# Optimization experiments

Measured on AMD Instinct MI355X. Metric: run time of the kernel, lower is better.

The kernel has to match this reference:

```python
import jax, jax.numpy as jnp
import numpy as np

N = 100000
E = 1600000
D = 128


def setup_inputs() -> dict:
    key = jax.random.key(0)
    k1, k2, k3 = jax.random.split(key, 3)
    indices = jax.random.randint(k1, (2, E), 0, N, dtype=jnp.int64)
    values = jax.random.normal(k2, (E,), dtype=jnp.float32)
    b = jax.random.normal(k3, (N, D), dtype=jnp.float32)
    return {"indices": indices, "values": values, "n": N, "b": b}


def reference(indices, values, n, b):
    # Sparse COO SpMM: out[r] = sum_{e: row[e]==r} values[e] * b[col[e]]
    row, col = indices[0], indices[1]
    contrib = values[:, None] * b[col]          # [E, D] gather-multiply
    out = jax.ops.segment_sum(contrib, row, num_segments=n)  # [N, D] scatter-add
    return out
```

## Files before the change

kernel.cpp:

```cpp
#include <hip/hip_runtime.h>
#include <hip/hip_fp16.h>


#define D_DIM 128
#define RPB 64
#define RPB_SHIFT 6
#define CRB 256
#define CRB_SHIFT 8
#define MAXCB 512
#define CCAP 4608
#define MAXB 2048
#define CAP_LDS 1408
#define EPT 6
#define EPT1 8
#define CHUNK1 4096
#define EPC 4
#define OVF_T 8192

typedef float fx4 __attribute__((ext_vector_type(4)));

__global__ __launch_bounds__(256) void convert_b_kernel(
        const float* __restrict__ b, __half* __restrict__ bh, int n8) {
    int i = blockIdx.x * blockDim.x + threadIdx.x;
    if (i >= n8) return;
    const float4* b4 = (const float4*)b;
    float4 a0 = b4[2 * i];
    float4 a1 = b4[2 * i + 1];
    union { __half2 h[4]; uint4 u; } pk;
    pk.h[0] = __floats2half2_rn(a0.x, a0.y);
    pk.h[1] = __floats2half2_rn(a0.z, a0.w);
    pk.h[2] = __floats2half2_rn(a1.x, a1.y);
    pk.h[3] = __floats2half2_rn(a1.z, a1.w);
    ((uint4*)bh)[i] = pk.u;
}

__global__ __launch_bounds__(1024) void p1_sortcoarse(
        const int* __restrict__ rows,
        const int* __restrict__ cols,
        const float* __restrict__ vals,
        int* __restrict__ coarse_cnt,
        int2* __restrict__ coarse,
        int* __restrict__ ovf_cnt,
        int* __restrict__ ovf3,
        int E, int ncb, int ccap) {
    __shared__ int hist[MAXCB];
    __shared__ int cursor[MAXCB];
    __shared__ int2 stage[CHUNK1];
    __shared__ unsigned short sbkt[CHUNK1];

    int tid = threadIdx.x;
    int start = blockIdx.x * CHUNK1;
    int end = start + CHUNK1; if (end > E) end = E;
    int n = end - start;

    for (int i = tid; i < ncb; i += 1024) hist[i] = 0;
    __syncthreads();

    int rr[EPC]; int cc[EPC]; float vv[EPC];
    int ne = 0;
    for (int e = start + tid; e < end; e += 1024) {
        int r = rows[e];
        if (ne < EPC) { rr[ne] = r; cc[ne] = cols[e]; vv[ne] = vals[e]; }
        ++ne;
        atomicAdd(&hist[r >> CRB_SHIFT], 1);
    }
    __syncthreads();

    for (int d = 1; d < ncb; d <<= 1) {
        int t = (tid < ncb && tid >= d) ? hist[tid - d] : 0;
        __syncthreads();
        if (tid < ncb && tid >= d) hist[tid] += t;
        __syncthreads();
    }

    int incl = 0, excl = 0;
    if (tid < ncb) { incl = hist[tid]; excl = tid ? hist[tid - 1] : 0; }
    __syncthreads();
    if (tid < ncb) {
        int cnt = incl - excl;
        cursor[tid] = excl;
        int gres = (cnt > 0) ? atomicAdd(&coarse_cnt[tid], cnt) : 0;
        hist[tid] = gres - excl;
    }
    __syncthreads();

    for (int j = 0; j < ne; ++j) {
        int r, c; float v;
        if (j < EPC) { r = rr[j]; c = cc[j]; v = vv[j]; }
        else { int e = start + tid + j * 1024; r = rows[e]; c = cols[e]; v = vals[e]; }
        int bkt = r >> CRB_SHIFT;
        int pos = atomicAdd(&cursor[bkt], 1);
        stage[pos] = make_int2(((r & (CRB - 1)) << 17) | c, __float_as_int(v));
        sbkt[pos] = (unsigned short)bkt;
    }
    __syncthreads();

    for (int i = tid; i < n; i += 1024) {
        int bkt = sbkt[i];
        int2 e = stage[i];
        int gidx = i + hist[bkt];
        if (gidx < ccap) {
            coarse[(size_t)bkt * ccap + gidx] = e;
        } else {
            int k = atomicAdd(ovf_cnt, 1);
            if (k < OVF_T) {
                int r = (bkt << CRB_SHIFT) | ((unsigned)e.x >> 17);
                ovf3[3 * k] = r; ovf3[3 * k + 1] = e.x & 0x1FFFF;
                ovf3[3 * k + 2] = e.y;
            }
        }
    }
}

__global__ __launch_bounds__(1024) void p2_fine(
        const int* __restrict__ coarse_cnt,
        const int2* __restrict__ coarse,
        int* __restrict__ bucket_cnt,
        int2* __restrict__ packed,
        int* __restrict__ ovf_cnt,
        int* __restrict__ ovf3,
        int ccap, int cap, int nb) {
    __shared__ int2 stage[CCAP];
    __shared__ int hist4[4];
    __shared__ int loff[5];
    __shared__ int cur[4];

    int bin = blockIdx.x;
    int tid = threadIdx.x;
    int lane = tid & 63;
    int cnt = coarse_cnt[bin];
    if (cnt > ccap) cnt = ccap;
    const int2* cb = coarse + (size_t)bin * ccap;

    if (tid < 4) hist4[tid] = 0;

    int h0 = 0, h1 = 0, h2 = 0, h3 = 0;
    for (int i = tid; i < cnt; i += 1024) {
        int f = (cb[i].x >> 23) & 3;
        h0 += (f == 0); h1 += (f == 1); h2 += (f == 2); h3 += (f == 3);
    }
    for (int off = 32; off; off >>= 1) {
        h0 += __shfl_down(h0, off); h1 += __shfl_down(h1, off);
        h2 += __shfl_down(h2, off); h3 += __shfl_down(h3, off);
    }
    __syncthreads();
    if (lane == 0) {
        atomicAdd(&hist4[0], h0); atomicAdd(&hist4[1], h1);
        atomicAdd(&hist4[2], h2); atomicAdd(&hist4[3], h3);
    }
    __syncthreads();
    if (tid == 0) {
        int o = 0;
        for (int k = 0; k < 4; ++k) { loff[k] = o; cur[k] = o; o += hist4[k]; }
        loff[4] = o;
    }
    __syncthreads();

    for (int i = tid; i < cnt; i += 1024) {
        int2 e = cb[i];
        int f = (e.x >> 23) & 3;
        int p = 0;
        for (int k = 0; k < 4; ++k) {
            unsigned long long m = __ballot(f == k);
            if (f == k) {
                int leader = __ffsll((unsigned long long)m) - 1;
                int base = 0;
                if (lane == leader) base = atomicAdd(&cur[k], (int)__popcll(m));
                base = __shfl(base, leader);
                p = base + (int)__popcll(m & ((1ULL << lane) - 1ULL));
            }
        }
        stage[p] = e;
    }
    __syncthreads();

    int fb0 = bin << (CRB_SHIFT - RPB_SHIFT);
    for (int k = 0; k < 4; ++k) {
        int bkt = fb0 + k;
        if (bkt >= nb) break;
        int s = loff[k];
        int run = loff[k + 1] - s;
        int w = (run > cap) ? cap : run;
        for (int i = tid; i < w; i += 1024) {
            int2 e = stage[s + i];
            packed[(size_t)bkt * cap + i] = make_int2(e.x & 0x7FFFFF, e.y);
        }
        if (tid == 0) bucket_cnt[bkt] = w;
        for (int i = cap + tid; i < run; i += 1024) {
            int2 e = stage[s + i];
            int k2 = atomicAdd(ovf_cnt, 1);
            if (k2 < OVF_T) {
                int r = (bin << CRB_SHIFT) | ((unsigned)e.x >> 17);
                ovf3[3 * k2] = r; ovf3[3 * k2 + 1] = e.x & 0x1FFFF;
                ovf3[3 * k2 + 2] = e.y;
            }
        }
    }
}

template <bool HALF>
__global__ __launch_bounds__(256) void phase2_sort_gather(
        const int* __restrict__ bucket_cnt,
        const int2* __restrict__ packed,
        const __half* __restrict__ bh,
        const float* __restrict__ b,
        float* __restrict__ out,
        int cap, int N) {
    __shared__ int2 sorted[CAP_LDS];
    __shared__ int hist[RPB];
    __shared__ int offs[RPB + 1];
    __shared__ int cursor[RPB];

    int bucket = blockIdx.x;
    int tid = threadIdx.x;

    int cnt = bucket_cnt[bucket];
    if (cnt > cap) cnt = cap;
    const int2* pk = packed + (size_t)bucket * cap;

    if (tid < RPB) hist[tid] = 0;
    __syncthreads();

    int2 ev[EPT];
    int  rl[EPT];
    int ne = 0;
    for (int i = tid; i < cnt; i += 256) {
        int2 e = pk[i];
        ev[ne] = e;
        rl[ne] = ((unsigned)e.x) >> 17;
        atomicAdd(&hist[rl[ne]], 1);
        ++ne;
    }
    __syncthreads();

    for (int d = 1; d < RPB; d <<= 1) {
        int t = (tid < RPB && tid >= d) ? hist[tid - d] : 0;
        __syncthreads();
        if (tid < RPB) hist[tid] += t;
        __syncthreads();
    }
    if (tid == 0) offs[0] = 0;
    if (tid < RPB) {
        offs[tid + 1] = hist[tid];
        cursor[tid] = (tid == 0) ? 0 : hist[tid - 1];
    }
    __syncthreads();

    for (int j = 0; j < ne; ++j) {
        int pos = atomicAdd(&cursor[rl[j]], 1);
        sorted[pos] = make_int2(ev[j].x & 0x1FFFF, ev[j].y);
    }
    __syncthreads();

    int g = tid >> 5;
    int glane = tid & 31;
    int r0 = bucket << RPB_SHIFT;
    for (int k = 0; k < 8; ++k) {
        int rr = g * 8 + k;
        int start = offs[rr];
        int num = offs[rr + 1] - start;
        float4 acc = make_float4(0.f, 0.f, 0.f, 0.f);
        for (int base = 0; base < num; base += 8) {
#pragma unroll
            for (int j = 0; j < 8; ++j) {
                int idx = base + j;
                int sidx = start + ((idx < num) ? idx : (num - 1));
                int2 e = sorted[sidx];
                float v = (idx < num) ? __int_as_float(e.y) : 0.f;
                if (HALF) {
                    uint2 hv = ((const uint2*)(bh + (size_t)e.x * D_DIM))[glane];
                    __half2* hp = (__half2*)&hv;
                    float2 f0 = __half22float2(hp[0]);
                    float2 f1 = __half22float2(hp[1]);
                    acc.x += v * f0.x;
                    acc.y += v * f0.y;
                    acc.z += v * f1.x;
                    acc.w += v * f1.y;
                } else {
                    float4 bv = ((const float4*)(b + (size_t)e.x * D_DIM))[glane];
                    acc.x += v * bv.x;
                    acc.y += v * bv.y;
                    acc.z += v * bv.z;
                    acc.w += v * bv.w;
                }
            }
        }
        int r = r0 + rr;
        if (r < N) {
            fx4 av = {acc.x, acc.y, acc.z, acc.w};
            __builtin_nontemporal_store(av, (fx4*)(out + (size_t)r * D_DIM) + glane);
        }
    }
}

__global__ __launch_bounds__(1024) void phase1_partition(
        const int* __restrict__ rows,
        const int* __restrict__ cols,
        const float* __restrict__ vals,
        int* __restrict__ bucket_cnt,
        int2* __restrict__ packed,
        int* __restrict__ ovf_cnt,
        int* __restrict__ ovf3,
        int E, int nb, int cap, int chunk) {
    __shared__ int hist[MAXB];
    int tid = threadIdx.x;
    int start = blockIdx.x * chunk;
    int end = start + chunk; if (end > E) end = E;

    for (int i = tid; i < nb; i += 1024) hist[i] = 0;
    __syncthreads();

    int rr[EPT1]; int cc[EPT1]; float vv[EPT1];
    int ne = 0;
    for (int e = start + tid; e < end; e += 1024) {
        int r = rows[e];
        if (ne < EPT1) { rr[ne] = r; cc[ne] = cols[e]; vv[ne] = vals[e]; }
        ++ne;
        atomicAdd(&hist[r >> RPB_SHIFT], 1);
    }
    __syncthreads();

    for (int bkt = tid; bkt < nb; bkt += 1024) {
        int c = hist[bkt];
        hist[bkt] = (c > 0) ? atomicAdd(&bucket_cnt[bkt], c) : 0;
    }
    __syncthreads();

    int j = 0;
    for (int e = start + tid; e < end; e += 1024, ++j) {
        int r, c; float v;
        if (j < EPT1) { r = rr[j]; c = cc[j]; v = vv[j]; }
        else          { r = rows[e]; c = cols[e]; v = vals[e]; }
        int bkt = r >> RPB_SHIFT;
        int local = atomicAdd(&hist[bkt], 1);
        if (local < cap) {
            int key = ((r & (RPB - 1)) << 17) | c;
            packed[(size_t)bkt * cap + local] = make_int2(key, __float_as_int(v));
        } else {
            int k = atomicAdd(ovf_cnt, 1);
            if (k < OVF_T) {
                ovf3[3 * k] = r; ovf3[3 * k + 1] = c;
                ovf3[3 * k + 2] = __float_as_int(v);
            }
        }
    }
}

__global__ void fixup_kernel(const int* __restrict__ ovf_cnt,
                             const int* __restrict__ ovf3,
                             const float* __restrict__ b,
                             float* __restrict__ out) {
    int items = *ovf_cnt;
    if (items > OVF_T) items = OVF_T;
    int gsz  = (gridDim.x * blockDim.x) >> 5;
    int gid  = (blockIdx.x * blockDim.x + threadIdx.x) >> 5;
    int lane = threadIdx.x & 31;
    for (int i = gid; i < items; i += gsz) {
        int r = ovf3[3 * i];
        int c = ovf3[3 * i + 1];
        float v = __int_as_float(ovf3[3 * i + 2]);
        float4 bv = ((const float4*)(b + (size_t)c * D_DIM))[lane];
        float* op = out + (size_t)r * D_DIM + (size_t)lane * 4;
        atomicAdd(op + 0, v * bv.x);
        atomicAdd(op + 1, v * bv.y);
        atomicAdd(op + 2, v * bv.z);
        atomicAdd(op + 3, v * bv.w);
    }
}

__global__ void spmm_atomic_kernel(const int* __restrict__ rows,
                                   const int* __restrict__ cols,
                                   const float* __restrict__ vals,
                                   const float* __restrict__ b,
                                   float* __restrict__ out, int E) {
    int t = blockIdx.x * blockDim.x + threadIdx.x;
    int e = t >> 5;
    if (e >= E) return;
    int lane = t & 31;
    int r = rows[e];
    int c = cols[e];
    float v = vals[e];
    float4 bv = ((const float4*)(b + (size_t)c * D_DIM))[lane];
    float* op = out + (size_t)r * D_DIM + (size_t)lane * 4;
    atomicAdd(op + 0, v * bv.x);
    atomicAdd(op + 1, v * bv.y);
    atomicAdd(op + 2, v * bv.z);
    atomicAdd(op + 3, v * bv.w);
}

extern "C" void kernel_launch(void* const* d_in, const int* in_sizes, int n_in,
                              void* d_out, int out_size, void* d_ws, size_t ws_size,
                              hipStream_t stream) {
    const int*   indices = (const int*)d_in[0];
    const float* vals    = (const float*)d_in[1];
    const float* b       = (const float*)d_in[3];
    float*       out     = (float*)d_out;

    int E = in_sizes[1];
    int N = out_size / D_DIM;
    const int* rows = indices;
    const int* cols = indices + E;

    int nb  = (N + RPB - 1) >> RPB_SHIFT;
    int ncb = (N + CRB - 1) >> CRB_SHIFT;
    int avg  = (nb  > 0) ? E / nb  : 0;
    int cavg = (ncb > 0) ? E / ncb : 0;
    int cap = CAP_LDS;
    size_t bh_bytes = (size_t)N * D_DIM * 2;
    int n8 = N * D_DIM / 8;

    {
        bool ok = (ncb <= MAXCB) && (N <= 131072) &&
                  (cavg + cavg / 8 <= CCAP) && (cap > avg + avg / 8);
        size_t fixedN = (size_t)ncb * 4 + (size_t)nb * 4 + 4 + (size_t)OVF_T * 12;
        size_t pk_off = (fixedN + 255) & ~(size_t)255;
        size_t un_off = (pk_off + (size_t)nb * cap * 8 + 255) & ~(size_t)255;
        size_t coarse_bytes = (size_t)ncb * CCAP * 8;
        size_t un_bytes = coarse_bytes > bh_bytes ? coarse_bytes : bh_bytes;
        if (ok && ws_size >= un_off + un_bytes) {
            char* w = (char*)d_ws;
            int*    coarse_cnt = (int*)w;
            int*    bucket_cnt = (int*)(w + (size_t)ncb * 4);
            int*    ovf_cnt    = (int*)(w + (size_t)ncb * 4 + (size_t)nb * 4);
            int*    ovf3       = (int*)(w + (size_t)ncb * 4 + (size_t)nb * 4 + 4);
            int2*   packed     = (int2*)(w + pk_off);
            int2*   coarse     = (int2*)(w + un_off);
            __half* bh         = (__half*)(w + un_off);

            (void)hipMemsetAsync(coarse_cnt, 0,
                                 (size_t)ncb * 4 + (size_t)nb * 4 + 4, stream);

            int nwg1 = (E + CHUNK1 - 1) / CHUNK1;
            p1_sortcoarse<<<nwg1, 1024, 0, stream>>>(
                rows, cols, vals, coarse_cnt, coarse, ovf_cnt, ovf3,
                E, ncb, CCAP);

            p2_fine<<<ncb, 1024, 0, stream>>>(
                coarse_cnt, coarse, bucket_cnt, packed, ovf_cnt, ovf3,
                CCAP, cap, nb);

            convert_b_kernel<<<(n8 + 255) / 256, 256, 0, stream>>>(b, bh, n8);

            phase2_sort_gather<true><<<nb, 256, 0, stream>>>(
                bucket_cnt, packed, bh, b, out, cap, N);

            fixup_kernel<<<8, 256, 0, stream>>>(ovf_cnt, ovf3, b, out);
            return;
        }
    }

    size_t fixed      = (size_t)nb * 4 + 4 + (size_t)OVF_T * 12;
    size_t bh_off     = (fixed + 255) & ~(size_t)255;
    size_t packed_h   = (bh_off + bh_bytes + 255) & ~(size_t)255;
    size_t packed_f   = bh_off;
    size_t need_h     = packed_h + (size_t)nb * cap * 8;
    size_t need_f     = packed_f + (size_t)nb * cap * 8;

    bool okBase = (nb <= MAXB) && (N <= 131072) && (cap > avg + avg / 8);
    bool useHalf = okBase && (ws_size >= need_h);
    bool useF32  = okBase && !useHalf && (ws_size >= need_f);

    if (!useHalf && !useF32) {
        (void)hipMemsetAsync(d_out, 0, (size_t)out_size * sizeof(float), stream);
        long long total = (long long)E * 32;
        int blocks = (int)((total + 255) / 256);
        spmm_atomic_kernel<<<blocks, 256, 0, stream>>>(rows, cols, vals, b, out, E);
        return;
    }

    char* w = (char*)d_ws;
    int*    bucket_cnt = (int*)w;
    int*    ovf_cnt    = (int*)(w + (size_t)nb * 4);
    int*    ovf3       = (int*)(w + (size_t)nb * 4 + 4);
    __half* bh         = (__half*)(w + bh_off);
    int2*   packed     = (int2*)(w + (useHalf ? packed_h : packed_f));

    (void)hipMemsetAsync(bucket_cnt, 0, (size_t)nb * 4 + 4, stream);

    if (useHalf)
        convert_b_kernel<<<(n8 + 255) / 256, 256, 0, stream>>>(b, bh, n8);

    const int P1_WGS = 256;
    int chunk = (E + P1_WGS - 1) / P1_WGS;
    phase1_partition<<<P1_WGS, 1024, 0, stream>>>(
        rows, cols, vals, bucket_cnt, packed, ovf_cnt, ovf3, E, nb, cap, chunk);

    if (useHalf)
        phase2_sort_gather<true><<<nb, 256, 0, stream>>>(
            bucket_cnt, packed, bh, b, out, cap, N);
    else
        phase2_sort_gather<false><<<nb, 256, 0, stream>>>(
            bucket_cnt, packed, bh, b, out, cap, N);

    fixup_kernel<<<8, 256, 0, stream>>>(ovf_cnt, ovf3, b, out);
}
```

Measured before the change: 216.9 us.

## Sort coarse bins into per-row CSR in place and gather rows directly

```diff
diff --git a/kernel.cpp b/kernel.cpp
--- a/kernel.cpp
+++ b/kernel.cpp
@@ -15,6 +15,7 @@
 #define EPT1 8
 #define CHUNK1 4096
 #define EPC 4
+#define EPC2 5
 #define OVF_T 8192
 
 typedef float fx4 __attribute__((ext_vector_type(4)));
@@ -112,87 +113,164 @@
     }
 }
 
-__global__ __launch_bounds__(1024) void p2_fine(
+__global__ __launch_bounds__(1024) void p2_rowsort(
         const int* __restrict__ coarse_cnt,
-        const int2* __restrict__ coarse,
+        int2* __restrict__ coarse,
+        int* __restrict__ row_beg,
+        int* __restrict__ row_num,
+        int ccap, int N) {
+    __shared__ int2 stage[CCAP];
+    __shared__ int hist[CRB];
+    __shared__ int offs[CRB + 1];
+    __shared__ int cursor[CRB];
+
+    int bin = blockIdx.x;
+    int tid = threadIdx.x;
+    int cnt = coarse_cnt[bin];
+    if (cnt > ccap) cnt = ccap;
+    int2* cb = coarse + (size_t)bin * ccap;
+
+    if (tid < CRB) hist[tid] = 0;
+    __syncthreads();
+
+    int2 ev[EPC2];
+    int  rl[EPC2];
+    int ne = 0;
+    for (int i = tid; i < cnt; i += 1024) {
+        int2 e = cb[i];
+        ev[ne] = e;
+        rl[ne] = ((unsigned)e.x) >> 17;
+        atomicAdd(&hist[rl[ne]], 1);
+        ++ne;
+    }
+    __syncthreads();
+
+    for (int d = 1; d < CRB; d <<= 1) {
+        int t = (tid < CRB && tid >= d) ? hist[tid - d] : 0;
+        __syncthreads();
+        if (tid < CRB) hist[tid] += (tid >= d) ? t : 0;
+        __syncthreads();
+    }
+    if (tid == 0) offs[0] = 0;
+    if (tid < CRB) {
+        offs[tid + 1] = hist[tid];
+        cursor[tid] = (tid == 0) ? 0 : hist[tid - 1];
+    }
+    __syncthreads();
+
+    for (int j = 0; j < ne; ++j) {
+        int pos = atomicAdd(&cursor[rl[j]], 1);
+        stage[pos] = make_int2(ev[j].x & 0x1FFFF, ev[j].y);
+    }
+    __syncthreads();
+
+    for (int i = tid; i < cnt; i += 1024) cb[i] = stage[i];
+    if (tid < CRB) {
+        int r = (bin << CRB_SHIFT) + tid;
+        if (r < N) {
+            row_beg[r] = bin * ccap + offs[tid];
+            row_num[r] = offs[tid + 1] - offs[tid];
+        }
+    }
+}
+
+template <bool HALF>
+__global__ __launch_bounds__(256) void csr_gather(
+        const int* __restrict__ row_beg,
+        const int* __restrict__ row_num,
+        const int2* __restrict__ csr,
+        const __half* __restrict__ bh,
+        const float* __restrict__ b,
+        float* __restrict__ out,
+        int N) {
+    int g = threadIdx.x >> 5;
+    int glane = threadIdx.x & 31;
+    int r = blockIdx.x * 8 + g;
+    if (r >= N) return;
+
+    int beg = row_beg[r];
+    int num = row_num[r];
+    const int2* pk = csr + beg;
+
+    float4 acc = make_float4(0.f, 0.f, 0.f, 0.f);
+    for (int base = 0; base < num; base += 8) {
+#pragma unroll
+        for (int j = 0; j < 8; ++j) {
+            int idx = base + j;
+            int sidx = (idx < num) ? idx : (num - 1);
+            int2 e = pk[sidx];
+            float v = (idx < num) ? __int_as_float(e.y) : 0.f;
+            if (HALF) {
+                uint2 hv = ((const uint2*)(bh + (size_t)e.x * D_DIM))[glane];
+                __half2* hp = (__half2*)&hv;
+                float2 f0 = __half22float2(hp[0]);
+                float2 f1 = __half22float2(hp[1]);
+                acc.x += v * f0.x;
+                acc.y += v * f0.y;
+                acc.z += v * f1.x;
+                acc.w += v * f1.y;
+            } else {
+                float4 bv = ((const float4*)(b + (size_t)e.x * D_DIM))[glane];
+                acc.x += v * bv.x;
+                acc.y += v * bv.y;
+                acc.z += v * bv.z;
+                acc.w += v * bv.w;
+            }
+        }
+    }
+    fx4 av = {acc.x, acc.y, acc.z, acc.w};
+    __builtin_nontemporal_store(av, (fx4*)(out + (size_t)r * D_DIM) + glane);
+}
+
+
+__global__ __launch_bounds__(1024) void phase1_partition(
+        const int* __restrict__ rows,
+        const int* __restrict__ cols,
+        const float* __restrict__ vals,
         int* __restrict__ bucket_cnt,
         int2* __restrict__ packed,
         int* __restrict__ ovf_cnt,
         int* __restrict__ ovf3,
-        int ccap, int cap, int nb) {
-    __shared__ int2 stage[CCAP];
-    __shared__ int hist4[4];
-    __shared__ int loff[5];
-    __shared__ int cur[4];
-
-    int bin = blockIdx.x;
+        int E, int nb, int cap, int chunk) {
+    __shared__ int hist[MAXB];
     int tid = threadIdx.x;
-    int lane = tid & 63;
-    int cnt = coarse_cnt[bin];
-    if (cnt > ccap) cnt = ccap;
-    const int2* cb = coarse + (size_t)bin * ccap;
-
-    if (tid < 4) hist4[tid] = 0;
-
-    int h0 = 0, h1 = 0, h2 = 0, h3 = 0;
-    for (int i = tid; i < cnt; i += 1024) {
-        int f = (cb[i].x >> 23) & 3;
-        h0 += (f == 0); h1 += (f == 1); h2 += (f == 2); h3 += (f == 3);
-    }
-    for (int off = 32; off; off >>= 1) {
-        h0 += __shfl_down(h0, off); h1 += __shfl_down(h1, off);
-        h2 += __shfl_down(h2, off); h3 += __shfl_down(h3, off);
-    }
-    __syncthreads();
-    if (lane == 0) {
-        atomicAdd(&hist4[0], h0); atomicAdd(&hist4[1], h1);
-        atomicAdd(&hist4[2], h2); atomicAdd(&hist4[3], h3);
-    }
-    __syncthreads();
-    if (tid == 0) {
-        int o = 0;
-        for (int k = 0; k < 4; ++k) { loff[k] = o; cur[k] = o; o += hist4[k]; }
-        loff[4] = o;
-    }
-    __syncthreads();
-
-    for (int i = tid; i < cnt; i += 1024) {
-        int2 e = cb[i];
-        int f = (e.x >> 23) & 3;
-        int p = 0;
-        for (int k = 0; k < 4; ++k) {
-            unsigned long long m = __ballot(f == k);
-            if (f == k) {
-                int leader = __ffsll((unsigned long long)m) - 1;
-                int base = 0;
-                if (lane == leader) base = atomicAdd(&cur[k], (int)__popcll(m));
-                base = __shfl(base, leader);
-                p = base + (int)__popcll(m & ((1ULL << lane) - 1ULL));
-            }
-        }
-        stage[p] = e;
-    }
-    __syncthreads();
-
-    int fb0 = bin << (CRB_SHIFT - RPB_SHIFT);
-    for (int k = 0; k < 4; ++k) {
-        int bkt = fb0 + k;
-        if (bkt >= nb) break;
-        int s = loff[k];
-        int run = loff[k + 1] - s;
-        int w = (run > cap) ? cap : run;
-        for (int i = tid; i < w; i += 1024) {
-            int2 e = stage[s + i];
-            packed[(size_t)bkt * cap + i] = make_int2(e.x & 0x7FFFFF, e.y);
-        }
-        if (tid == 0) bucket_cnt[bkt] = w;
-        for (int i = cap + tid; i < run; i += 1024) {
-            int2 e = stage[s + i];
-            int k2 = atomicAdd(ovf_cnt, 1);
-            if (k2 < OVF_T) {
-                int r = (bin << CRB_SHIFT) | ((unsigned)e.x >> 17);
-                ovf3[3 * k2] = r; ovf3[3 * k2 + 1] = e.x & 0x1FFFF;
-                ovf3[3 * k2 + 2] = e.y;
+    int start = blockIdx.x * chunk;
+    int end = start + chunk; if (end > E) end = E;
+
+    for (int i = tid; i < nb; i += 1024) hist[i] = 0;
+    __syncthreads();
+
+    int rr[EPT1]; int cc[EPT1]; float vv[EPT1];
+    int ne = 0;
+    for (int e = start + tid; e < end; e += 1024) {
+        int r = rows[e];
+        if (ne < EPT1) { rr[ne] = r; cc[ne] = cols[e]; vv[ne] = vals[e]; }
+        ++ne;
+        atomicAdd(&hist[r >> RPB_SHIFT], 1);
+    }
+    __syncthreads();
+
+    for (int bkt = tid; bkt < nb; bkt += 1024) {
+        int c = hist[bkt];
+        hist[bkt] = (c > 0) ? atomicAdd(&bucket_cnt[bkt], c) : 0;
+    }
+    __syncthreads();
+
+    int j = 0;
+    for (int e = start + tid; e < end; e += 1024, ++j) {
+        int r, c; float v;
+        if (j < EPT1) { r = rr[j]; c = cc[j]; v = vv[j]; }
+        else          { r = rows[e]; c = cols[e]; v = vals[e]; }
+        int bkt = r >> RPB_SHIFT;
+        int local = atomicAdd(&hist[bkt], 1);
+        if (local < cap) {
+            int key = ((r & (RPB - 1)) << 17) | c;
+            packed[(size_t)bkt * cap + local] = make_int2(key, __float_as_int(v));
+        } else {
+            int k = atomicAdd(ovf_cnt, 1);
+            if (k < OVF_T) {
+                ovf3[3 * k] = r; ovf3[3 * k + 1] = c;
+                ovf3[3 * k + 2] = __float_as_int(v);
             }
         }
     }
@@ -293,59 +371,6 @@
     }
 }
 
-__global__ __launch_bounds__(1024) void phase1_partition(
-        const int* __restrict__ rows,
-        const int* __restrict__ cols,
-        const float* __restrict__ vals,
-        int* __restrict__ bucket_cnt,
-        int2* __restrict__ packed,
-        int* __restrict__ ovf_cnt,
-        int* __restrict__ ovf3,
-        int E, int nb, int cap, int chunk) {
-    __shared__ int hist[MAXB];
-    int tid = threadIdx.x;
-    int start = blockIdx.x * chunk;
-    int end = start + chunk; if (end > E) end = E;
-
-    for (int i = tid; i < nb; i += 1024) hist[i] = 0;
-    __syncthreads();
-
-    int rr[EPT1]; int cc[EPT1]; float vv[EPT1];
-    int ne = 0;
-    for (int e = start + tid; e < end; e += 1024) {
-        int r = rows[e];
-        if (ne < EPT1) { rr[ne] = r; cc[ne] = cols[e]; vv[ne] = vals[e]; }
-        ++ne;
-        atomicAdd(&hist[r >> RPB_SHIFT], 1);
-    }
-    __syncthreads();
-
-    for (int bkt = tid; bkt < nb; bkt += 1024) {
-        int c = hist[bkt];
-        hist[bkt] = (c > 0) ? atomicAdd(&bucket_cnt[bkt], c) : 0;
-    }
-    __syncthreads();
-
-    int j = 0;
-    for (int e = start + tid; e < end; e += 1024, ++j) {
-        int r, c; float v;
-        if (j < EPT1) { r = rr[j]; c = cc[j]; v = vv[j]; }
-        else          { r = rows[e]; c = cols[e]; v = vals[e]; }
-        int bkt = r >> RPB_SHIFT;
-        int local = atomicAdd(&hist[bkt], 1);
-        if (local < cap) {
-            int key = ((r & (RPB - 1)) << 17) | c;
-            packed[(size_t)bkt * cap + local] = make_int2(key, __float_as_int(v));
-        } else {
-            int k = atomicAdd(ovf_cnt, 1);
-            if (k < OVF_T) {
-                ovf3[3 * k] = r; ovf3[3 * k + 1] = c;
-                ovf3[3 * k + 2] = __float_as_int(v);
-            }
-        }
-    }
-}
-
 __global__ void fixup_kernel(const int* __restrict__ ovf_cnt,
                              const int* __restrict__ ovf3,
                              const float* __restrict__ b,
@@ -405,50 +430,49 @@
     int ncb = (N + CRB - 1) >> CRB_SHIFT;
     int avg  = (nb  > 0) ? E / nb  : 0;
     int cavg = (ncb > 0) ? E / ncb : 0;
-    int cap = CAP_LDS;
     size_t bh_bytes = (size_t)N * D_DIM * 2;
     int n8 = N * D_DIM / 8;
 
     {
-        bool ok = (ncb <= MAXCB) && (N <= 131072) &&
-                  (cavg + cavg / 8 <= CCAP) && (cap > avg + avg / 8);
-        size_t fixedN = (size_t)ncb * 4 + (size_t)nb * 4 + 4 + (size_t)OVF_T * 12;
-        size_t pk_off = (fixedN + 255) & ~(size_t)255;
-        size_t un_off = (pk_off + (size_t)nb * cap * 8 + 255) & ~(size_t)255;
-        size_t coarse_bytes = (size_t)ncb * CCAP * 8;
-        size_t un_bytes = coarse_bytes > bh_bytes ? coarse_bytes : bh_bytes;
-        if (ok && ws_size >= un_off + un_bytes) {
+        bool ok = (ncb <= MAXCB) && (N <= 131072) && (cavg + cavg / 8 <= CCAP);
+        size_t rb_off = (size_t)ncb * 4;
+        size_t rn_off = rb_off + (size_t)N * 4;
+        size_t oc_off = rn_off + (size_t)N * 4;
+        size_t o3_off = oc_off + 4;
+        size_t co_off = (o3_off + (size_t)OVF_T * 12 + 255) & ~(size_t)255;
+        size_t bh_off = (co_off + (size_t)ncb * CCAP * 8 + 255) & ~(size_t)255;
+        if (ok && ws_size >= bh_off + bh_bytes) {
             char* w = (char*)d_ws;
             int*    coarse_cnt = (int*)w;
-            int*    bucket_cnt = (int*)(w + (size_t)ncb * 4);
-            int*    ovf_cnt    = (int*)(w + (size_t)ncb * 4 + (size_t)nb * 4);
-            int*    ovf3       = (int*)(w + (size_t)ncb * 4 + (size_t)nb * 4 + 4);
-            int2*   packed     = (int2*)(w + pk_off);
-            int2*   coarse     = (int2*)(w + un_off);
-            __half* bh         = (__half*)(w + un_off);
-
-            (void)hipMemsetAsync(coarse_cnt, 0,
-                                 (size_t)ncb * 4 + (size_t)nb * 4 + 4, stream);
+            int*    row_beg    = (int*)(w + rb_off);
+            int*    row_num    = (int*)(w + rn_off);
+            int*    ovf_cnt    = (int*)(w + oc_off);
+            int*    ovf3       = (int*)(w + o3_off);
+            int2*   coarse     = (int2*)(w + co_off);
+            __half* bh         = (__half*)(w + bh_off);
+
+            (void)hipMemsetAsync(coarse_cnt, 0, (size_t)ncb * 4, stream);
+            (void)hipMemsetAsync(ovf_cnt, 0, 4, stream);
 
             int nwg1 = (E + CHUNK1 - 1) / CHUNK1;
             p1_sortcoarse<<<nwg1, 1024, 0, stream>>>(
                 rows, cols, vals, coarse_cnt, coarse, ovf_cnt, ovf3,
                 E, ncb, CCAP);
 
-            p2_fine<<<ncb, 1024, 0, stream>>>(
-                coarse_cnt, coarse, bucket_cnt, packed, ovf_cnt, ovf3,
-                CCAP, cap, nb);
+            p2_rowsort<<<ncb, 1024, 0, stream>>>(
+                coarse_cnt, coarse, row_beg, row_num, CCAP, N);
 
             convert_b_kernel<<<(n8 + 255) / 256, 256, 0, stream>>>(b, bh, n8);
 
-            phase2_sort_gather<true><<<nb, 256, 0, stream>>>(
-                bucket_cnt, packed, bh, b, out, cap, N);
+            csr_gather<true><<<(N + 7) / 8, 256, 0, stream>>>(
+                row_beg, row_num, coarse, bh, b, out, N);
 
             fixup_kernel<<<8, 256, 0, stream>>>(ovf_cnt, ovf3, b, out);
             return;
         }
     }
 
+    int cap = CAP_LDS;
     size_t fixed      = (size_t)nb * 4 + 4 + (size_t)OVF_T * 12;
     size_t bh_off     = (fixed + 255) & ~(size_t)255;
     size_t packed_h   = (bh_off + bh_bytes + 255) & ~(size_t)255;
```

After: 232.9 us. 1.07x slower.
